# Kernel tuning notes

Measured on AMD Instinct MI355X. Metric: run time of the kernel, lower is better.

Reference implementation:

```python
import jax, jax.numpy as jnp
import numpy as np

N_NODES = 65536
N_EDGES = 786432
N_RELS = 8
IN_DIM = 128
HID = 128
N_CLASSES = 10
N_GRAPHS = 64


def setup_inputs() -> dict:
    key = jax.random.key(0)
    ks = jax.random.split(key, 10)
    h = jax.random.normal(ks[0], (N_NODES, IN_DIM), dtype=jnp.float32)
    s = 1.0 / np.sqrt(IN_DIM)
    W1 = jax.random.normal(ks[1], (N_RELS, IN_DIM, HID), dtype=jnp.float32) * s
    W1_self = jax.random.normal(ks[2], (IN_DIM, HID), dtype=jnp.float32) * s
    b1 = jnp.zeros((HID,), dtype=jnp.float32)
    sh = 1.0 / np.sqrt(HID)
    W2 = jax.random.normal(ks[3], (N_RELS, HID, HID), dtype=jnp.float32) * sh
    W2_self = jax.random.normal(ks[4], (HID, HID), dtype=jnp.float32) * sh
    b2 = jnp.zeros((HID,), dtype=jnp.float32)
    Wc = jax.random.normal(ks[5], (HID, N_CLASSES), dtype=jnp.float32) * sh
    bc = jnp.zeros((N_CLASSES,), dtype=jnp.float32)
    src = jax.random.randint(ks[6], (N_EDGES,), 0, N_NODES, dtype=jnp.int32)
    dst = jax.random.randint(ks[7], (N_EDGES,), 0, N_NODES, dtype=jnp.int32)
    etype = jax.random.randint(ks[8], (N_EDGES,), 0, N_RELS, dtype=jnp.int32)
    # 64 batched graphs of 1024 nodes each (contiguous node blocks)
    graph_ids = (jnp.arange(N_NODES, dtype=jnp.int32) // (N_NODES // N_GRAPHS)).astype(jnp.int32)
    return dict(h=h, W1=W1, W1_self=W1_self, b1=b1, W2=W2, W2_self=W2_self,
                b2=b2, Wc=Wc, bc=bc, src=src, dst=dst, etype=etype,
                graph_ids=graph_ids)


def _relgraphconv(h, W, W_self, b, src, dst, etype):
    # DGL RelGraphConv (regularizer=None, self_loop=True, bias=True, no norm):
    # out[v] = sum_{e: dst(e)=v} W[etype(e)] @ h[src(e)]  +  W_self @ h[v] + b
    # Transform all nodes under each relation (R is small), then gather per-edge.
    xw = jnp.einsum('ni,rio->rno', h, W)          # [R, N, HID]
    msg = xw[etype, src]                           # [E, HID] gather
    agg = jax.ops.segment_sum(msg, dst, num_segments=N_NODES)  # scatter-add
    return agg + h @ W_self + b


def reference(h, W1, W1_self, b1, W2, W2_self, b2, Wc, bc,
              src, dst, etype, graph_ids):
    h1 = jax.nn.relu(_relgraphconv(h, W1, W1_self, b1, src, dst, etype))
    h2 = jax.nn.relu(_relgraphconv(h1, W2, W2_self, b2, src, dst, etype))
    pooled = jax.ops.segment_max(h2, graph_ids, num_segments=N_GRAPHS)  # [G, HID]
    return pooled @ Wc + bc
```

## Files before the change

kernel.cpp:

```cpp
#include <hip/hip_runtime.h>
#include <hip/hip_bf16.h>


#define N_NODES 65536
#define N_EDGES 786432
#define DIM 128
#define NT 9
#define XW_LD (NT * DIM)
#define N_GRAPHS 64
#define G_GEMM 4608
#define G_FUSED 10752

typedef unsigned int uint;
typedef unsigned short ushort;
typedef __attribute__((ext_vector_type(8))) short short8;
typedef __attribute__((ext_vector_type(4))) float f32x4;

__device__ inline ushort f2b(float f) {
  uint u = __float_as_uint(f);
  u += 0x7fff + ((u >> 16) & 1);
  return (ushort)(u >> 16);
}
__device__ inline float b2f(ushort h) { return __uint_as_float(((uint)h) << 16); }
__device__ inline float blo(uint v) { return __uint_as_float(v << 16); }
__device__ inline float bhi(uint v) { return __uint_as_float(v & 0xffff0000u); }

__device__ inline void gl_lds16(const void* g, void* l) {
  __builtin_amdgcn_global_load_lds(
      (const __attribute__((address_space(1))) unsigned int*)g,
      (__attribute__((address_space(3))) unsigned int*)l, 16, 0, 0);
}

__global__ __launch_bounds__(256) void prep(const float* __restrict__ h,
                                            ushort* __restrict__ hb,
                                            const float* __restrict__ W1,
                                            const float* __restrict__ W1s,
                                            const float* __restrict__ W2,
                                            const float* __restrict__ W2s,
                                            ushort* __restrict__ Wt1,
                                            ushort* __restrict__ Wt2) {
  const int bid = blockIdx.x, tid = threadIdx.x;
  if (bid < 8192) {
    int i = bid * 256 + tid;
    float4 v = ((const float4*)h)[i];
    ushort4 o;
    o.x = f2b(v.x); o.y = f2b(v.y); o.z = f2b(v.z); o.w = f2b(v.w);
    ((ushort4*)hb)[i] = o;
  } else {
    int b = bid - 8192;
    const float* S;
    ushort* D;
    int tile;
    if (b < 9) { D = Wt1; tile = b; S = (b < 8) ? (W1 + (size_t)b * 16384) : W1s; }
    else       { D = Wt2; tile = b - 9; S = (tile < 8) ? (W2 + (size_t)tile * 16384) : W2s; }
    for (int i = tid; i < 16384; i += 256) {
      int n = i >> 7, k = i & 127;
      D[((size_t)tile * 128 + n) * 128 + k] = f2b(S[k * 128 + n]);
    }
  }
}

__device__ __forceinline__ void gemm_body(const ushort* __restrict__ A,
                                          const ushort* __restrict__ Bt,
                                          ushort* __restrict__ C, int ldc,
                                          int tile, char* lds) {
  const int bm = tile / 9, bn = tile % 9;
  const char* Ag = (const char*)(A + (size_t)bm * 128 * 128);
  const char* Bg = (const char*)(Bt + (size_t)bn * 128 * 128);
  const int tid = threadIdx.x, wv = tid >> 6, ln = tid & 63;
  const int wm = wv >> 1, wn = wv & 1, lr = ln & 15, kq = ln >> 4;

  f32x4 acc[4][4];
#pragma unroll
  for (int m = 0; m < 4; ++m)
#pragma unroll
    for (int n = 0; n < 4; ++n) acc[m][n] = (f32x4){0.f, 0.f, 0.f, 0.f};

#pragma unroll
  for (int kt = 0; kt < 2; ++kt) {
    if (kt) __syncthreads();
#pragma unroll
    for (int it = 0; it < 4; ++it) {
      int chunk = it * 4096 + wv * 1024;
      int p = chunk + ln * 16;
      int row = p >> 7, inb = p & 127;
      int sw = inb ^ ((row & 7) << 4);
      size_t gb = (size_t)row * 256 + (size_t)kt * 128 + sw;
      gl_lds16(Ag + gb, lds + chunk);
      gl_lds16(Bg + gb, lds + 16384 + chunk);
    }
    asm volatile("s_waitcnt vmcnt(0)" ::: "memory");
    __syncthreads();
#pragma unroll
    for (int k2 = 0; k2 < 2; ++k2) {
      const int kb = k2 * 64 + kq * 16;
      short8 a[4], b[4];
#pragma unroll
      for (int m = 0; m < 4; ++m) {
        int row = wm * 64 + m * 16 + lr;
        a[m] = *(const short8*)(lds + ((row * 128 + kb) ^ ((row & 7) << 4)));
      }
#pragma unroll
      for (int n = 0; n < 4; ++n) {
        int col = wn * 64 + n * 16 + lr;
        b[n] = *(const short8*)(lds + 16384 + ((col * 128 + kb) ^ ((col & 7) << 4)));
      }
#pragma unroll
      for (int m = 0; m < 4; ++m)
#pragma unroll
        for (int n = 0; n < 4; ++n)
          acc[m][n] = __builtin_amdgcn_mfma_f32_16x16x32_bf16(a[m], b[n], acc[m][n], 0, 0, 0);
    }
  }

  __syncthreads();
#pragma unroll
  for (int m = 0; m < 4; ++m) {
    int rb0 = wm * 64 + m * 16 + kq * 4;
#pragma unroll
    for (int n = 0; n < 4; ++n) {
      int col = wn * 64 + n * 16 + lr;
#pragma unroll
      for (int e = 0; e < 4; ++e) {
        int row = rb0 + e;
        int off = (row * 256 + col * 2) ^ ((row & 7) << 4);
        *(ushort*)(lds + off) = f2b(acc[m][n][e]);
      }
    }
  }
  __syncthreads();
  char* Cg = (char*)C + (size_t)(bm * 128) * (size_t)ldc * 2 + (size_t)bn * 256;
#pragma unroll
  for (int it = 0; it < 8; ++it) {
    int p = it * 4096 + tid * 16;
    int row = p >> 8, inb = p & 255;
    short8 v = *(const short8*)(lds + row * 256 + (inb ^ ((row & 7) << 4)));
    *(short8*)(Cg + (size_t)row * (size_t)ldc * 2 + inb) = v;
  }
}

__global__ __launch_bounds__(256, 4) void gemm_bk64(const ushort* __restrict__ A,
                                                    const ushort* __restrict__ Bt,
                                                    ushort* __restrict__ C, int ldc) {
  __shared__ char lds[32768];
  gemm_body(A, Bt, C, ldc, (blockIdx.x & 7) * 576 + (blockIdx.x >> 3), lds);
}

__global__ __launch_bounds__(256, 4) void gemm1_fill(const ushort* __restrict__ A,
                                                     const ushort* __restrict__ Bt,
                                                     ushort* __restrict__ C, int ldc,
                                                     const int* __restrict__ src,
                                                     const int* __restrict__ dst,
                                                     const int* __restrict__ et,
                                                     int* __restrict__ cnt,
                                                     uint* __restrict__ bins) {
  __shared__ char lds[32768];
  const int bid = blockIdx.x;
  const int xcd = bid & 7, s = bid >> 3;
  const int q = s / 7, r = s % 7;
  if (r < 3) {
    gemm_body(A, Bt, C, ldc, xcd * 576 + q * 3 + r, lds);
    return;
  }
  const int f = q * 4 + (r - 3);
  const int e0 = f * 1024 + threadIdx.x * 4;
  int4 d4 = *(const int4*)(dst + e0);
  int4 s4 = *(const int4*)(src + e0);
  int4 t4 = *(const int4*)(et + e0);
  uint r0 = (uint)s4.x * 576u + (uint)t4.x * 64u;
  uint r1 = (uint)s4.y * 576u + (uint)t4.y * 64u;
  uint r2 = (uint)s4.z * 576u + (uint)t4.z * 64u;
  uint r3 = (uint)s4.w * 576u + (uint)t4.w * 64u;
  if ((d4.x >> 13) == xcd) {
    int rk = atomicAdd(&cnt[d4.x], 1);
    if (rk < 64) bins[((size_t)d4.x << 6) + rk] = r0;
  }
  if ((d4.y >> 13) == xcd) {
    int rk = atomicAdd(&cnt[d4.y], 1);
    if (rk < 64) bins[((size_t)d4.y << 6) + rk] = r1;
  }
  if ((d4.z >> 13) == xcd) {
    int rk = atomicAdd(&cnt[d4.z], 1);
    if (rk < 64) bins[((size_t)d4.z << 6) + rk] = r2;
  }
  if ((d4.w >> 13) == xcd) {
    int rk = atomicAdd(&cnt[d4.w], 1);
    if (rk < 64) bins[((size_t)d4.w << 6) + rk] = r3;
  }
}

template <bool POOL>
__global__ __launch_bounds__(256) void gather_out(const uint* __restrict__ XWu,
                                                  const uint* __restrict__ bins,
                                                  const int* __restrict__ cnt,
                                                  const float* __restrict__ bias,
                                                  uint* __restrict__ hout,
                                                  ushort* __restrict__ partial2) {
  __shared__ ushort pm[4][128];
  int node = (blockIdx.x * 256 + threadIdx.x) >> 6;
  int w = threadIdx.x >> 6;
  int ln = threadIdx.x & 63;
  int ne = __builtin_amdgcn_readfirstlane(cnt[node]);
  if (ne > 64) ne = 64;
  uint sv = XWu[(size_t)node * 576 + 512 + ln];
  float2 bv = ((const float2*)bias)[ln];
  uint mv = bins[((size_t)node << 6) + ln];
  float2 acc = {0.f, 0.f};

  for (int c = 0; c < ne; c += 16) {
    uint v[16];
#pragma unroll
    for (int j = 0; j < 16; ++j) {
      int i = c + j;
      int idx = (i < ne) ? i : (ne - 1);
      uint off = (uint)__builtin_amdgcn_readlane((int)mv, idx);
      v[j] = XWu[off + ln];
    }
#pragma unroll
    for (int j = 0; j < 16; ++j) {
      uint m = (c + j < ne) ? 0xffffffffu : 0u;
      uint x = v[j] & m;
      acc.x += blo(x);
      acc.y += bhi(x);
    }
  }

  float r0 = fmaxf(acc.x + blo(sv) + bv.x, 0.f);
  float r1 = fmaxf(acc.y + bhi(sv) + bv.y, 0.f);
  if (POOL) {
    pm[w][ln * 2] = f2b(r0);
    pm[w][ln * 2 + 1] = f2b(r1);
    __syncthreads();
    int t = threadIdx.x;
    if (t < 128) {
      float m = fmaxf(fmaxf(b2f(pm[0][t]), b2f(pm[1][t])),
                      fmaxf(b2f(pm[2][t]), b2f(pm[3][t])));
      partial2[(size_t)blockIdx.x * 128 + t] = f2b(m);
    }
  } else {
    hout[(size_t)node * 64 + ln] = (uint)f2b(r0) | ((uint)f2b(r1) << 16);
  }
}

__global__ __launch_bounds__(256) void classify2(const ushort* __restrict__ partial2,
                                                 const float* __restrict__ Wc,
                                                 const float* __restrict__ bc,
                                                 float* __restrict__ out) {
  __shared__ float red[2][128];
  __shared__ float pooled[128];
  int g = blockIdx.x, t = threadIdx.x;
  int d = t & 127, half = t >> 7;
  const ushort* base = partial2 + ((size_t)g * 256 + half * 128) * 128;
  float m = 0.f;
  for (int i = 0; i < 128; ++i) m = fmaxf(m, b2f(base[i * 128 + d]));
  red[half][d] = m;
  __syncthreads();
  if (t < 128) pooled[t] = fmaxf(red[0][t], red[1][t]);
  __syncthreads();
  if (t < 10) {
    float s = bc[t];
    for (int dd = 0; dd < DIM; ++dd) s += pooled[dd] * Wc[dd * 10 + t];
    out[g * 10 + t] = s;
  }
}

extern "C" void kernel_launch(void* const* d_in, const int* in_sizes, int n_in,
                              void* d_out, int out_size, void* d_ws, size_t ws_size,
                              hipStream_t stream) {
  const float* h       = (const float*)d_in[0];
  const float* W1      = (const float*)d_in[1];
  const float* W1_self = (const float*)d_in[2];
  const float* b1      = (const float*)d_in[3];
  const float* W2      = (const float*)d_in[4];
  const float* W2_self = (const float*)d_in[5];
  const float* b2      = (const float*)d_in[6];
  const float* Wc      = (const float*)d_in[7];
  const float* bc      = (const float*)d_in[8];
  const int* src   = (const int*)d_in[9];
  const int* dst   = (const int*)d_in[10];
  const int* etype = (const int*)d_in[11];
  float* out = (float*)d_out;

  char* ws = (char*)d_ws;
  ushort* XW      = (ushort*)(ws);
  ushort* hb      = (ushort*)(ws + 150994944);
  ushort* h1b     = (ushort*)(ws + 167772160);
  ushort* Wt1c    = (ushort*)(ws + 184549376);
  ushort* Wt2c    = (ushort*)(ws + 184844288);
  int*    cnt     = (int*)(ws + 185139200);
  uint*   bins    = (uint*)(ws + 185401344);
  ushort* partial2= (ushort*)(ws + 202178560);

  const int g_gather = N_NODES / 4;

  hipMemsetAsync(cnt, 0, N_NODES * sizeof(int), stream);
  prep<<<8192 + 18, 256, 0, stream>>>(h, hb, W1, W1_self, W2, W2_self, Wt1c, Wt2c);

  gemm1_fill<<<G_FUSED, 256, 0, stream>>>(hb, Wt1c, XW, XW_LD,
                                          src, dst, etype, cnt, bins);
  gather_out<false><<<g_gather, 256, 0, stream>>>((const uint*)XW, bins, cnt, b1,
                                                  (uint*)h1b, partial2);

  gemm_bk64<<<G_GEMM, 256, 0, stream>>>(h1b, Wt2c, XW, XW_LD);
  gather_out<true><<<g_gather, 256, 0, stream>>>((const uint*)XW, bins, cnt, b2,
                                                 (uint*)h1b, partial2);

  classify2<<<N_GRAPHS, 256, 0, stream>>>(partial2, Wc, bc, out);

  (void)in_sizes; (void)n_in; (void)out_size; (void)ws_size;
}
```

Before: 229.2 us.

## Store layer-2 transformed features in FP8 and rewrite gather loops

The second-layer GEMM now writes its per-relation transformed node features as FP8 e4m3 instead of bf16, which halves the bytes the layer-2 gather and pool kernel must read per edge. The gather kernels are also split into bf16 and fp8 variants, and the masked 16-wide batch loop is replaced by an unrolled 8/4/1 edge loop without padding loads. The aim is to cut memory traffic for the large intermediate and the wasted loads. The cost is lower precision in the layer-2 messages, which risks accuracy tolerance, and possibly less memory-level parallelism from the shorter unroll.

Result: faster. 207.2 us, median of 3 (-9.6%).

```diff
diff --git a/kernel.cpp b/kernel.cpp
--- a/kernel.cpp
+++ b/kernel.cpp
@@ -1,5 +1,6 @@
 #include <hip/hip_runtime.h>
 #include <hip/hip_bf16.h>
+#include <hip/hip_fp8.h>
 
 
 #define N_NODES 65536
@@ -7,12 +8,14 @@
 #define DIM 128
 #define NT 9
 #define XW_LD (NT * DIM)
+#define XW_LDB 1152
 #define N_GRAPHS 64
 #define G_GEMM 4608
 #define G_FUSED 10752
 
 typedef unsigned int uint;
 typedef unsigned short ushort;
+typedef unsigned char uchar;
 typedef __attribute__((ext_vector_type(8))) short short8;
 typedef __attribute__((ext_vector_type(4))) float f32x4;
 
@@ -24,6 +27,16 @@
 __device__ inline float b2f(ushort h) { return __uint_as_float(((uint)h) << 16); }
 __device__ inline float blo(uint v) { return __uint_as_float(v << 16); }
 __device__ inline float bhi(uint v) { return __uint_as_float(v & 0xffff0000u); }
+
+__device__ inline uchar f2fp8(float f) {
+  __hip_fp8_e4m3 q(f);
+  return (uchar)q.__x;
+}
+__device__ inline float fp82f(uchar b) {
+  __hip_fp8_e4m3 q;
+  q.__x = b;
+  return (float)q;
+}
 
 __device__ inline void gl_lds16(const void* g, void* l) {
   __builtin_amdgcn_global_load_lds(
@@ -60,22 +73,10 @@
   }
 }
 
-__device__ __forceinline__ void gemm_body(const ushort* __restrict__ A,
-                                          const ushort* __restrict__ Bt,
-                                          ushort* __restrict__ C, int ldc,
-                                          int tile, char* lds) {
-  const int bm = tile / 9, bn = tile % 9;
-  const char* Ag = (const char*)(A + (size_t)bm * 128 * 128);
-  const char* Bg = (const char*)(Bt + (size_t)bn * 128 * 128);
+__device__ __forceinline__ void gemm_core(const char* Ag, const char* Bg,
+                                          char* lds, f32x4 (*acc)[4]) {
   const int tid = threadIdx.x, wv = tid >> 6, ln = tid & 63;
   const int wm = wv >> 1, wn = wv & 1, lr = ln & 15, kq = ln >> 4;
-
-  f32x4 acc[4][4];
-#pragma unroll
-  for (int m = 0; m < 4; ++m)
-#pragma unroll
-    for (int n = 0; n < 4; ++n) acc[m][n] = (f32x4){0.f, 0.f, 0.f, 0.f};
-
 #pragma unroll
   for (int kt = 0; kt < 2; ++kt) {
     if (kt) __syncthreads();
@@ -112,6 +113,22 @@
           acc[m][n] = __builtin_amdgcn_mfma_f32_16x16x32_bf16(a[m], b[n], acc[m][n], 0, 0, 0);
     }
   }
+}
+
+__device__ __forceinline__ void gemm_body_bf16(const ushort* __restrict__ A,
+                                               const ushort* __restrict__ Bt,
+                                               ushort* __restrict__ C,
+                                               int tile, char* lds) {
+  const int bm = tile / 9, bn = tile % 9;
+  const int tid = threadIdx.x, wv = tid >> 6, ln = tid & 63;
+  const int wm = wv >> 1, wn = wv & 1, lr = ln & 15, kq = ln >> 4;
+  f32x4 acc[4][4];
+#pragma unroll
+  for (int m = 0; m < 4; ++m)
+#pragma unroll
+    for (int n = 0; n < 4; ++n) acc[m][n] = (f32x4){0.f, 0.f, 0.f, 0.f};
+  gemm_core((const char*)(A + (size_t)bm * 128 * 128),
+            (const char*)(Bt + (size_t)bn * 128 * 128), lds, acc);
 
   __syncthreads();
 #pragma unroll
@@ -129,26 +146,61 @@
     }
   }
   __syncthreads();
-  char* Cg = (char*)C + (size_t)(bm * 128) * (size_t)ldc * 2 + (size_t)bn * 256;
+  char* Cg = (char*)C + (size_t)(bm * 128) * XW_LD * 2 + (size_t)bn * 256;
 #pragma unroll
   for (int it = 0; it < 8; ++it) {
     int p = it * 4096 + tid * 16;
     int row = p >> 8, inb = p & 255;
     short8 v = *(const short8*)(lds + row * 256 + (inb ^ ((row & 7) << 4)));
-    *(short8*)(Cg + (size_t)row * (size_t)ldc * 2 + inb) = v;
-  }
-}
-
-__global__ __launch_bounds__(256, 4) void gemm_bk64(const ushort* __restrict__ A,
-                                                    const ushort* __restrict__ Bt,
-                                                    ushort* __restrict__ C, int ldc) {
+    *(short8*)(Cg + (size_t)row * XW_LD * 2 + inb) = v;
+  }
+}
+
+__global__ __launch_bounds__(256, 4) void gemm_bk64_fp8(const ushort* __restrict__ A,
+                                                        const ushort* __restrict__ Bt,
+                                                        uchar* __restrict__ C) {
   __shared__ char lds[32768];
-  gemm_body(A, Bt, C, ldc, (blockIdx.x & 7) * 576 + (blockIdx.x >> 3), lds);
+  const int tile = (blockIdx.x & 7) * 576 + (blockIdx.x >> 3);
+  const int bm = tile / 9, bn = tile % 9;
+  const int tid = threadIdx.x, wv = tid >> 6, ln = tid & 63;
+  const int wm = wv >> 1, wn = wv & 1, lr = ln & 15, kq = ln >> 4;
+  f32x4 acc[4][4];
+#pragma unroll
+  for (int m = 0; m < 4; ++m)
+#pragma unroll
+    for (int n = 0; n < 4; ++n) acc[m][n] = (f32x4){0.f, 0.f, 0.f, 0.f};
+  gemm_core((const char*)(A + (size_t)bm * 128 * 128),
+            (const char*)(Bt + (size_t)bn * 128 * 128), lds, acc);
+
+  __syncthreads();
+#pragma unroll
+  for (int m = 0; m < 4; ++m) {
+    int rb0 = wm * 64 + m * 16 + kq * 4;
+#pragma unroll
+    for (int n = 0; n < 4; ++n) {
+      int col = wn * 64 + n * 16 + lr;
+#pragma unroll
+      for (int e = 0; e < 4; ++e) {
+        int row = rb0 + e;
+        int off = (row * 128 + col) ^ ((row & 7) << 4);
+        *(uchar*)(lds + off) = f2fp8(acc[m][n][e]);
+      }
+    }
+  }
+  __syncthreads();
+  uchar* Cg = C + (size_t)(bm * 128) * XW_LDB + (size_t)bn * 128;
+#pragma unroll
+  for (int it = 0; it < 4; ++it) {
+    int p = it * 4096 + tid * 16;
+    int row = p >> 7, inb = p & 127;
+    short8 v = *(const short8*)(lds + row * 128 + (inb ^ ((row & 7) << 4)));
+    *(short8*)(Cg + (size_t)row * XW_LDB + inb) = v;
+  }
 }
 
 __global__ __launch_bounds__(256, 4) void gemm1_fill(const ushort* __restrict__ A,
                                                      const ushort* __restrict__ Bt,
-                                                     ushort* __restrict__ C, int ldc,
+                                                     ushort* __restrict__ C,
                                                      const int* __restrict__ src,
                                                      const int* __restrict__ dst,
                                                      const int* __restrict__ et,
@@ -159,7 +211,7 @@
   const int xcd = bid & 7, s = bid >> 3;
   const int q = s / 7, r = s % 7;
   if (r < 3) {
-    gemm_body(A, Bt, C, ldc, xcd * 576 + q * 3 + r, lds);
+    gemm_body_bf16(A, Bt, C, xcd * 576 + q * 3 + r, lds);
     return;
   }
   const int f = q * 4 + (r - 3);
@@ -189,16 +241,12 @@
   }
 }
 
-template <bool POOL>
-__global__ __launch_bounds__(256) void gather_out(const uint* __restrict__ XWu,
-                                                  const uint* __restrict__ bins,
-                                                  const int* __restrict__ cnt,
-                                                  const float* __restrict__ bias,
-                                                  uint* __restrict__ hout,
-                                                  ushort* __restrict__ partial2) {
-  __shared__ ushort pm[4][128];
+__global__ __launch_bounds__(256) void gather_bf16(const uint* __restrict__ XWu,
+                                                   const uint* __restrict__ bins,
+                                                   const int* __restrict__ cnt,
+                                                   const float* __restrict__ bias,
+                                                   uint* __restrict__ hout) {
   int node = (blockIdx.x * 256 + threadIdx.x) >> 6;
-  int w = threadIdx.x >> 6;
   int ln = threadIdx.x & 63;
   int ne = __builtin_amdgcn_readfirstlane(cnt[node]);
   if (ne > 64) ne = 64;
@@ -207,38 +255,72 @@
   uint mv = bins[((size_t)node << 6) + ln];
   float2 acc = {0.f, 0.f};
 
-  for (int c = 0; c < ne; c += 16) {
-    uint v[16];
-#pragma unroll
-    for (int j = 0; j < 16; ++j) {
-      int i = c + j;
-      int idx = (i < ne) ? i : (ne - 1);
-      uint off = (uint)__builtin_amdgcn_readlane((int)mv, idx);
-      v[j] = XWu[off + ln];
-    }
-#pragma unroll
-    for (int j = 0; j < 16; ++j) {
-      uint m = (c + j < ne) ? 0xffffffffu : 0u;
-      uint x = v[j] & m;
-      acc.x += blo(x);
-      acc.y += bhi(x);
-    }
-  }
+#define EDGE(ii)                                                              \
+  do {                                                                        \
+    uint off = (uint)__builtin_amdgcn_readlane((int)mv, (ii));                \
+    uint v_ = XWu[off + ln];                                                  \
+    acc.x += blo(v_); acc.y += bhi(v_);                                       \
+  } while (0)
+  int i = 0;
+  for (; i + 8 <= ne; i += 8) {
+    EDGE(i + 0); EDGE(i + 1); EDGE(i + 2); EDGE(i + 3);
+    EDGE(i + 4); EDGE(i + 5); EDGE(i + 6); EDGE(i + 7);
+  }
+  for (; i + 4 <= ne; i += 4) {
+    EDGE(i + 0); EDGE(i + 1); EDGE(i + 2); EDGE(i + 3);
+  }
+  for (; i < ne; ++i) EDGE(i);
+#undef EDGE
 
   float r0 = fmaxf(acc.x + blo(sv) + bv.x, 0.f);
   float r1 = fmaxf(acc.y + bhi(sv) + bv.y, 0.f);
-  if (POOL) {
-    pm[w][ln * 2] = f2b(r0);
-    pm[w][ln * 2 + 1] = f2b(r1);
-    __syncthreads();
-    int t = threadIdx.x;
-    if (t < 128) {
-      float m = fmaxf(fmaxf(b2f(pm[0][t]), b2f(pm[1][t])),
-                      fmaxf(b2f(pm[2][t]), b2f(pm[3][t])));
-      partial2[(size_t)blockIdx.x * 128 + t] = f2b(m);
-    }
-  } else {
-    hout[(size_t)node * 64 + ln] = (uint)f2b(r0) | ((uint)f2b(r1) << 16);
+  hout[(size_t)node * 64 + ln] = (uint)f2b(r0) | ((uint)f2b(r1) << 16);
+}
+
+__global__ __launch_bounds__(256) void gather_fp8_pool(const uchar* __restrict__ XW8,
+                                                       const uint* __restrict__ bins,
+                                                       const int* __restrict__ cnt,
+                                                       const float* __restrict__ bias,
+                                                       ushort* __restrict__ partial2) {
+  __shared__ ushort pm[4][128];
+  int node = (blockIdx.x * 256 + threadIdx.x) >> 6;
+  int w = threadIdx.x >> 6;
+  int ln = threadIdx.x & 63;
+  int ne = __builtin_amdgcn_readfirstlane(cnt[node]);
+  if (ne > 64) ne = 64;
+  ushort sv = *(const ushort*)(XW8 + (size_t)node * XW_LDB + 1024 + ln * 2);
+  float2 bv = ((const float2*)bias)[ln];
+  uint mv = bins[((size_t)node << 6) + ln];
+  float2 acc = {0.f, 0.f};
+
+#define EDGE(ii)                                                              \
+  do {                                                                        \
+    uint off = (uint)__builtin_amdgcn_readlane((int)mv, (ii));                \
+    ushort wv_ = *(const ushort*)(XW8 + (size_t)off * 2 + ln * 2);            \
+    acc.x += fp82f((uchar)(wv_ & 0xff));                                      \
+    acc.y += fp82f((uchar)(wv_ >> 8));                                        \
+  } while (0)
+  int i = 0;
+  for (; i + 8 <= ne; i += 8) {
+    EDGE(i + 0); EDGE(i + 1); EDGE(i + 2); EDGE(i + 3);
+    EDGE(i + 4); EDGE(i + 5); EDGE(i + 6); EDGE(i + 7);
+  }
+  for (; i + 4 <= ne; i += 4) {
+    EDGE(i + 0); EDGE(i + 1); EDGE(i + 2); EDGE(i + 3);
+  }
+  for (; i < ne; ++i) EDGE(i);
+#undef EDGE
+
+  float r0 = fmaxf(acc.x + fp82f((uchar)(sv & 0xff)) + bv.x, 0.f);
+  float r1 = fmaxf(acc.y + fp82f((uchar)(sv >> 8)) + bv.y, 0.f);
+  pm[w][ln * 2] = f2b(r0);
+  pm[w][ln * 2 + 1] = f2b(r1);
+  __syncthreads();
+  int t = threadIdx.x;
+  if (t < 128) {
+    float m = fmaxf(fmaxf(b2f(pm[0][t]), b2f(pm[1][t])),
+                    fmaxf(b2f(pm[2][t]), b2f(pm[3][t])));
+    partial2[(size_t)blockIdx.x * 128 + t] = f2b(m);
   }
 }
 
@@ -283,6 +365,7 @@
 
   char* ws = (char*)d_ws;
   ushort* XW      = (ushort*)(ws);
+  uchar*  XW8     = (uchar*)(ws);
   ushort* hb      = (ushort*)(ws + 150994944);
   ushort* h1b     = (ushort*)(ws + 167772160);
   ushort* Wt1c    = (ushort*)(ws + 184549376);
@@ -296,14 +379,13 @@
   hipMemsetAsync(cnt, 0, N_NODES * sizeof(int), stream);
   prep<<<8192 + 18, 256, 0, stream>>>(h, hb, W1, W1_self, W2, W2_self, Wt1c, Wt2c);
 
-  gemm1_fill<<<G_FUSED, 256, 0, stream>>>(hb, Wt1c, XW, XW_LD,
+  gemm1_fill<<<G_FUSED, 256, 0, stream>>>(hb, Wt1c, XW,
                                           src, dst, etype, cnt, bins);
-  gather_out<false><<<g_gather, 256, 0, stream>>>((const uint*)XW, bins, cnt, b1,
-                                                  (uint*)h1b, partial2);
-
-  gemm_bk64<<<G_GEMM, 256, 0, stream>>>(h1b, Wt2c, XW, XW_LD);
-  gather_out<true><<<g_gather, 256, 0, stream>>>((const uint*)XW, bins, cnt, b2,
-                                                 (uint*)h1b, partial2);
+  gather_bf16<<<g_gather, 256, 0, stream>>>((const uint*)XW, bins, cnt, b1,
+                                            (uint*)h1b);
+
+  gemm_bk64_fp8<<<G_GEMM, 256, 0, stream>>>(h1b, Wt2c, XW8);
+  gather_fp8_pool<<<g_gather, 256, 0, stream>>>(XW8, bins, cnt, b2, partial2);
 
   classify2<<<N_GRAPHS, 256, 0, stream>>>(partial2, Wc, bc, out);
 
```
